# Kernel tuning notes

Measured on AMD Instinct MI355X. Metric: run time of the kernel, lower is better.

## Reference

```python
import jax, jax.numpy as jnp
import numpy as np

# Fixed genome topology (layered DAG, topologically ordered levels)
B = 4096      # batch
N_IN = 512    # input nodes
H1 = 1536     # hidden level 1
H2 = 1536     # hidden level 2
N_OUT = 512   # output nodes
FAN = 32      # fan-in per non-input node


def setup_inputs() -> dict:
    key = jax.random.key(0)
    ks = jax.random.split(key, 10)
    x = jax.random.normal(ks[0], (B, N_IN), dtype=jnp.float32)
    # level 1: sources among inputs [0, N_IN)
    src0 = jax.random.randint(ks[1], (H1 * FAN,), 0, N_IN, dtype=jnp.int32)
    dst0 = jax.random.randint(ks[2], (H1 * FAN,), 0, H1, dtype=jnp.int32)
    w0 = jax.random.normal(ks[3], (H1 * FAN,), dtype=jnp.float32) * 0.1
    # level 2: sources among inputs + level1 [0, N_IN+H1)
    src1 = jax.random.randint(ks[4], (H2 * FAN,), 0, N_IN + H1, dtype=jnp.int32)
    dst1 = jax.random.randint(ks[5], (H2 * FAN,), 0, H2, dtype=jnp.int32)
    w1 = jax.random.normal(ks[6], (H2 * FAN,), dtype=jnp.float32) * 0.1
    # output level: sources among all earlier nodes [0, N_IN+H1+H2)
    src2 = jax.random.randint(ks[7], (N_OUT * FAN,), 0, N_IN + H1 + H2, dtype=jnp.int32)
    dst2 = jax.random.randint(ks[8], (N_OUT * FAN,), 0, N_OUT, dtype=jnp.int32)
    w2 = jax.random.normal(ks[9], (N_OUT * FAN,), dtype=jnp.float32) * 0.1
    return dict(x=x, src0=src0, dst0=dst0, w0=w0,
                src1=src1, dst1=dst1, w1=w1,
                src2=src2, dst2=dst2, w2=w2)


def _level(node_values, src, dst, w, size):
    # per-edge weighted gather: [B, E]
    vals = node_values[:, src] * w
    # scatter-add into destination nodes of this level: [B, size]
    agg = jnp.zeros((node_values.shape[0], size), node_values.dtype).at[:, dst].add(vals)
    # per-node activation (genome.activation == 'relu'); relu(0)=0 matches
    # original's behavior of leaving unconnected nodes at zero
    return jax.nn.relu(agg)


def reference(x, src0, dst0, w0, src1, dst1, w1, src2, dst2, w2):
    nv = x                                        # [B, N_IN]
    h1 = _level(nv, src0, dst0, w0, H1)           # [B, H1]
    nv = jnp.concatenate([nv, h1], axis=1)        # [B, N_IN+H1]
    h2 = _level(nv, src1, dst1, w1, H2)           # [B, H2]
    nv = jnp.concatenate([nv, h2], axis=1)        # [B, N_IN+H1+H2]
    out = _level(nv, src2, dst2, w2, N_OUT)       # [B, N_OUT]
    return out
```

## Files before the change

### kernel.cpp

```cpp
#include <hip/hip_runtime.h>
#include <hip/hip_fp16.h>
#include <stdint.h>

#define BATCH 4096
#define N_IN  512
#define H1    1536
#define H2    1536
#define N_OUT 512
#define E0 (H1 * 32)
#define E1 (H2 * 32)
#define E2 (N_OUT * 32)
#define ETOT (E0 + E1 + E2)
#define NNODES (H1 + H2 + N_OUT)
#define MAXDEG 128

#define OFF_EDGES 33554432
#define OFF_CNT   (OFF_EDGES + (size_t)NNODES * MAXDEG * 8)

__global__ __launch_bounds__(256) void k_transpose_in(const float* __restrict__ x,
                                                      __half* __restrict__ xT) {
    __shared__ float tile[32][33];
    const int tx = threadIdx.x, ty = threadIdx.y;
    const int n0 = blockIdx.x * 32;
    const int b0 = blockIdx.y * 32;
#pragma unroll
    for (int k = 0; k < 32; k += 8)
        tile[ty + k][tx] = x[(size_t)(b0 + ty + k) * N_IN + (n0 + tx)];
    __syncthreads();
#pragma unroll
    for (int k = 0; k < 32; k += 8)
        xT[(size_t)(n0 + ty + k) * BATCH + (b0 + tx)] = __float2half_rn(tile[tx][ty + k]);
}

__global__ __launch_bounds__(256) void k_fill(const int* __restrict__ s0, const int* __restrict__ d0, const float* __restrict__ w0,
                                              const int* __restrict__ s1, const int* __restrict__ d1, const float* __restrict__ w1,
                                              const int* __restrict__ s2, const int* __restrict__ d2, const float* __restrict__ w2,
                                              int* __restrict__ cnt, int2* __restrict__ edges) {
    const int e = blockIdx.x * 256 + threadIdx.x;
    int src, node; float w;
    if (e < E0)           { src = s0[e];          node = d0[e];                w = w0[e]; }
    else if (e < E0 + E1) { int i = e - E0;       src = s1[i]; node = H1 + d1[i];        w = w1[i]; }
    else                  { int i = e - E0 - E1;  src = s2[i]; node = H1 + H2 + d2[i];   w = w2[i]; }
    const int pos = atomicAdd(&cnt[node], 1);
    if (pos < MAXDEG) edges[(size_t)node * MAXDEG + pos] = make_int2(src, __float_as_int(w));
}

__global__ __launch_bounds__(256) void k_pad(const int* __restrict__ cnt,
                                             int2* __restrict__ edges) {
    const int i = blockIdx.x * 256 + threadIdx.x;
    const int node = i >> 3, p = i & 7;
    if (node >= NNODES) return;
    int c = cnt[node];
    c = (c < 0) ? 0 : (c > MAXDEG - 8 ? MAXDEG - 8 : c);
    edges[(size_t)node * MAXDEG + c + p] = make_int2(0, 0);
}

__global__ __launch_bounds__(256, 2)
void k_level(const int2* __restrict__ edges,
             const int* __restrict__ cnt,
             const uint4* __restrict__ nv,
             uint4* __restrict__ outb) {
    const int tid  = threadIdx.x;
    const int lane = tid & 63, wv = tid >> 6;
    const int node = (blockIdx.y << 2) | wv;
    const int col8 = ((int)blockIdx.x << 6) | lane;

    int c = cnt[node];
    c = (c < 0) ? 0 : (c > MAXDEG - 8 ? MAXDEG - 8 : c);
    const int cp = (c + 7) & ~7;

    float a0 = 0.f, a1 = 0.f, a2 = 0.f, a3 = 0.f, a4 = 0.f, a5 = 0.f, a6 = 0.f, a7 = 0.f;
    const int2* slot = edges + (size_t)node * MAXDEG;

#define LOADK(k)                                                               \
    const int   s##k = __builtin_amdgcn_readlane(my.x, j + k) & 4095;          \
    const float w##k = __int_as_float(__builtin_amdgcn_readlane(my.y, j + k)); \
    const uint4 q##k = nv[((size_t)s##k << 9) | col8];

#define ACCK(k) {                                                  \
    const __half2* h = (const __half2*)&q##k;                      \
    a0 = fmaf(__low2float(h[0]),  w##k, a0);                       \
    a1 = fmaf(__high2float(h[0]), w##k, a1);                       \
    a2 = fmaf(__low2float(h[1]),  w##k, a2);                       \
    a3 = fmaf(__high2float(h[1]), w##k, a3);                       \
    a4 = fmaf(__low2float(h[2]),  w##k, a4);                       \
    a5 = fmaf(__high2float(h[2]), w##k, a5);                       \
    a6 = fmaf(__low2float(h[3]),  w##k, a6);                       \
    a7 = fmaf(__high2float(h[3]), w##k, a7); }

    for (int base = 0; base < cp; base += 64) {
        const int2 my = slot[base + lane];
        const int m = (cp - base < 64) ? (cp - base) : 64;
        for (int j = 0; j < m; j += 8) {
            LOADK(0) LOADK(1) LOADK(2) LOADK(3)
            LOADK(4) LOADK(5) LOADK(6) LOADK(7)
            ACCK(0) ACCK(1) ACCK(2) ACCK(3)
            ACCK(4) ACCK(5) ACCK(6) ACCK(7)
        }
    }
#undef LOADK
#undef ACCK

    a0 = fmaxf(a0, 0.f); a1 = fmaxf(a1, 0.f); a2 = fmaxf(a2, 0.f); a3 = fmaxf(a3, 0.f);
    a4 = fmaxf(a4, 0.f); a5 = fmaxf(a5, 0.f); a6 = fmaxf(a6, 0.f); a7 = fmaxf(a7, 0.f);

    const __half2 h0 = __floats2half2_rn(a0, a1);
    const __half2 h1 = __floats2half2_rn(a2, a3);
    const __half2 h2 = __floats2half2_rn(a4, a5);
    const __half2 h3 = __floats2half2_rn(a6, a7);
    uint4 p;
    p.x = *(const uint32_t*)&h0; p.y = *(const uint32_t*)&h1;
    p.z = *(const uint32_t*)&h2; p.w = *(const uint32_t*)&h3;
    outb[((size_t)node << 9) | col8] = p;
}

__global__ __launch_bounds__(256) void k_transpose_out(const __half* __restrict__ outh,
                                                       float* __restrict__ out) {
    __shared__ float tile[32][33];
    const int tx = threadIdx.x, ty = threadIdx.y;
    const int n0 = blockIdx.x * 32;
    const int b0 = blockIdx.y * 32;
#pragma unroll
    for (int k = 0; k < 32; k += 8)
        tile[ty + k][tx] = __half2float(outh[(size_t)(n0 + ty + k) * BATCH + (b0 + tx)]);
    __syncthreads();
#pragma unroll
    for (int k = 0; k < 32; k += 8)
        out[(size_t)(b0 + ty + k) * N_OUT + (n0 + tx)] = tile[tx][ty + k];
}

extern "C" void kernel_launch(void* const* d_in, const int* in_sizes, int n_in,
                              void* d_out, int out_size, void* d_ws, size_t ws_size,
                              hipStream_t stream) {
    const float* x  = (const float*)d_in[0];
    const int* s0   = (const int*)d_in[1];
    const int* dd0  = (const int*)d_in[2];
    const float* w0 = (const float*)d_in[3];
    const int* s1   = (const int*)d_in[4];
    const int* dd1  = (const int*)d_in[5];
    const float* w1 = (const float*)d_in[6];
    const int* s2   = (const int*)d_in[7];
    const int* dd2  = (const int*)d_in[8];
    const float* w2 = (const float*)d_in[9];

    char*   ws    = (char*)d_ws;
    __half* nvh   = (__half*)ws;
    uint4*  nv4   = (uint4*)ws;
    int2*   edges = (int2*)(ws + OFF_EDGES);
    int*    cnt   = (int*)(ws + OFF_CNT);

    hipMemsetAsync(cnt, 0, NNODES * sizeof(int), stream);
    k_fill<<<ETOT / 256, 256, 0, stream>>>(s0, dd0, w0, s1, dd1, w1, s2, dd2, w2, cnt, edges);
    k_pad<<<(NNODES * 8 + 255) / 256, 256, 0, stream>>>(cnt, edges);

    k_transpose_in<<<dim3(N_IN / 32, BATCH / 32), dim3(32, 8), 0, stream>>>(x, nvh);

    k_level<<<dim3(8, H1 / 4), 256, 0, stream>>>(edges, cnt, nv4,
                                                 nv4 + (size_t)N_IN * 512);
    k_level<<<dim3(8, H2 / 4), 256, 0, stream>>>(edges + (size_t)H1 * MAXDEG, cnt + H1, nv4,
                                                 nv4 + (size_t)(N_IN + H1) * 512);
    k_level<<<dim3(8, N_OUT / 4), 256, 0, stream>>>(edges + (size_t)(H1 + H2) * MAXDEG, cnt + H1 + H2, nv4,
                                                    nv4 + (size_t)(N_IN + H1 + H2) * 512);

    k_transpose_out<<<dim3(N_OUT / 32, BATCH / 32), dim3(32, 8), 0, stream>>>(
        (const __half*)(ws + (size_t)(N_IN + H1 + H2) * BATCH * 2), (float*)d_out);
}
```

Baseline: 151.4 us.

## Fuse all three levels into one batch-tiled kernel with node values in LDS

Replaces the transpose, per-level gather kernels and output transpose with a single kernel where each block owns 16 batch rows and keeps every node's fp16 values in shared memory across all three levels. Edges are packed into 32-bit words (16-bit source, fp16 weight) in fixed 80-slot rows, and the zero padding comes from memsetting the whole edge buffer. The intent is to remove the global-memory round trips for intermediate activations and the separate launches. In exchange, weights are rounded to fp16, in-degree is capped at 80, and the large LDS footprint (about 114 KB per block) limits occupancy and may cause bank conflicts on the gathered reads.

```diff
diff --git a/kernel.cpp b/kernel.cpp
--- a/kernel.cpp
+++ b/kernel.cpp
@@ -12,121 +12,96 @@
 #define E2 (N_OUT * 32)
 #define ETOT (E0 + E1 + E2)
 #define NNODES (H1 + H2 + N_OUT)
-#define MAXDEG 128
+#define PDEG 80
+#define C    16
 
-#define OFF_EDGES 33554432
-#define OFF_CNT   (OFF_EDGES + (size_t)NNODES * MAXDEG * 8)
+#define EDGE_BYTES ((size_t)NNODES * PDEG * 4)
+#define OFF_CNT    EDGE_BYTES
 
-__global__ __launch_bounds__(256) void k_transpose_in(const float* __restrict__ x,
-                                                      __half* __restrict__ xT) {
-    __shared__ float tile[32][33];
-    const int tx = threadIdx.x, ty = threadIdx.y;
-    const int n0 = blockIdx.x * 32;
-    const int b0 = blockIdx.y * 32;
-#pragma unroll
-    for (int k = 0; k < 32; k += 8)
-        tile[ty + k][tx] = x[(size_t)(b0 + ty + k) * N_IN + (n0 + tx)];
-    __syncthreads();
-#pragma unroll
-    for (int k = 0; k < 32; k += 8)
-        xT[(size_t)(n0 + ty + k) * BATCH + (b0 + tx)] = __float2half_rn(tile[tx][ty + k]);
+__global__ __launch_bounds__(256) void k_fill4(const int* __restrict__ s0, const int* __restrict__ d0, const float* __restrict__ w0,
+                                               const int* __restrict__ s1, const int* __restrict__ d1, const float* __restrict__ w1,
+                                               const int* __restrict__ s2, const int* __restrict__ d2, const float* __restrict__ w2,
+                                               int* __restrict__ cnt, uint32_t* __restrict__ edge4) {
+    const int e = blockIdx.x * 256 + threadIdx.x;
+    int src, node; float w;
+    if (e < E0)           { src = s0[e];          node = d0[e];                 w = w0[e]; }
+    else if (e < E0 + E1) { int i = e - E0;       src = s1[i]; node = H1 + d1[i];         w = w1[i]; }
+    else                  { int i = e - E0 - E1;  src = s2[i]; node = H1 + H2 + d2[i];    w = w2[i]; }
+    const int pos = atomicAdd(&cnt[node], 1);
+    if (pos < PDEG) {
+        const uint32_t hw = (uint32_t)__half_as_ushort(__float2half_rn(w));
+        edge4[(size_t)node * PDEG + pos] = ((uint32_t)src & 0xffffu) | (hw << 16);
+    }
 }
 
-__global__ __launch_bounds__(256) void k_fill(const int* __restrict__ s0, const int* __restrict__ d0, const float* __restrict__ w0,
-                                              const int* __restrict__ s1, const int* __restrict__ d1, const float* __restrict__ w1,
-                                              const int* __restrict__ s2, const int* __restrict__ d2, const float* __restrict__ w2,
-                                              int* __restrict__ cnt, int2* __restrict__ edges) {
-    const int e = blockIdx.x * 256 + threadIdx.x;
-    int src, node; float w;
-    if (e < E0)           { src = s0[e];          node = d0[e];                w = w0[e]; }
-    else if (e < E0 + E1) { int i = e - E0;       src = s1[i]; node = H1 + d1[i];        w = w1[i]; }
-    else                  { int i = e - E0 - E1;  src = s2[i]; node = H1 + H2 + d2[i];   w = w2[i]; }
-    const int pos = atomicAdd(&cnt[node], 1);
-    if (pos < MAXDEG) edges[(size_t)node * MAXDEG + pos] = make_int2(src, __float_as_int(w));
-}
+__global__ __launch_bounds__(512, 2)
+void k_net(const float* __restrict__ x,
+           const uint32_t* __restrict__ edge4,
+           const int* __restrict__ cnt,
+           float* __restrict__ out) {
+    __shared__ __half nvl[NNODES * C];
+    const int tid  = threadIdx.x;
+    const int b0   = blockIdx.x * C;
+    const int wave = tid >> 6, lane = tid & 63;
+    const int sub  = lane >> 3;
+    const int cp   = lane & 7;
 
-__global__ __launch_bounds__(256) void k_pad(const int* __restrict__ cnt,
-                                             int2* __restrict__ edges) {
-    const int i = blockIdx.x * 256 + threadIdx.x;
-    const int node = i >> 3, p = i & 7;
-    if (node >= NNODES) return;
-    int c = cnt[node];
-    c = (c < 0) ? 0 : (c > MAXDEG - 8 ? MAXDEG - 8 : c);
-    edges[(size_t)node * MAXDEG + c + p] = make_int2(0, 0);
-}
+#pragma unroll 4
+    for (int i = 0; i < C; ++i)
+        nvl[tid * C + i] = __float2half_rn(x[(size_t)(b0 + i) * N_IN + tid]);
+    __syncthreads();
 
-__global__ __launch_bounds__(256, 2)
-void k_level(const int2* __restrict__ edges,
-             const int* __restrict__ cnt,
-             const uint4* __restrict__ nv,
-             uint4* __restrict__ outb) {
-    const int tid  = threadIdx.x;
-    const int lane = tid & 63, wv = tid >> 6;
-    const int node = (blockIdx.y << 2) | wv;
-    const int col8 = ((int)blockIdx.x << 6) | lane;
+#pragma unroll 1
+    for (int l = 0; l < 3; ++l) {
+        const int nocts  = (l == 2) ? (N_OUT >> 3) : (H1 >> 3);
+        const int ebase  = (l == 0) ? 0 : (l == 1) ? H1 : (H1 + H2);
+        const int nvbase = (l == 0) ? N_IN : (N_IN + H1);
 
-    int c = cnt[node];
-    c = (c < 0) ? 0 : (c > MAXDEG - 8 ? MAXDEG - 8 : c);
-    const int cp = (c + 7) & ~7;
+        for (int o = wave; o < nocts; o += 8) {
+            const int ln   = (o << 3) | sub;
+            const int node = ebase + ln;
+            int c = cnt[node];
+            c = (c < 0) ? 0 : (c > PDEG ? PDEG : c);
+            int qm = c;
+#pragma unroll
+            for (int s = 8; s < 64; s += 8) {
+                const int oc = __builtin_amdgcn_readlane(c, s);
+                qm = (oc > qm) ? oc : qm;
+            }
+            qm = __builtin_amdgcn_readlane(qm, 0);
+            const int qmax = (qm + 7) & ~7;
 
-    float a0 = 0.f, a1 = 0.f, a2 = 0.f, a3 = 0.f, a4 = 0.f, a5 = 0.f, a6 = 0.f, a7 = 0.f;
-    const int2* slot = edges + (size_t)node * MAXDEG;
-
-#define LOADK(k)                                                               \
-    const int   s##k = __builtin_amdgcn_readlane(my.x, j + k) & 4095;          \
-    const float w##k = __int_as_float(__builtin_amdgcn_readlane(my.y, j + k)); \
-    const uint4 q##k = nv[((size_t)s##k << 9) | col8];
-
-#define ACCK(k) {                                                  \
-    const __half2* h = (const __half2*)&q##k;                      \
-    a0 = fmaf(__low2float(h[0]),  w##k, a0);                       \
-    a1 = fmaf(__high2float(h[0]), w##k, a1);                       \
-    a2 = fmaf(__low2float(h[1]),  w##k, a2);                       \
-    a3 = fmaf(__high2float(h[1]), w##k, a3);                       \
-    a4 = fmaf(__low2float(h[2]),  w##k, a4);                       \
-    a5 = fmaf(__high2float(h[2]), w##k, a5);                       \
-    a6 = fmaf(__low2float(h[3]),  w##k, a6);                       \
-    a7 = fmaf(__high2float(h[3]), w##k, a7); }
-
-    for (int base = 0; base < cp; base += 64) {
-        const int2 my = slot[base + lane];
-        const int m = (cp - base < 64) ? (cp - base) : 64;
-        for (int j = 0; j < m; j += 8) {
-            LOADK(0) LOADK(1) LOADK(2) LOADK(3)
-            LOADK(4) LOADK(5) LOADK(6) LOADK(7)
-            ACCK(0) ACCK(1) ACCK(2) ACCK(3)
-            ACCK(4) ACCK(5) ACCK(6) ACCK(7)
+            const uint32_t* __restrict__ row = edge4 + (size_t)node * PDEG;
+            float a0 = 0.f, a1 = 0.f;
+            uint4 e0 = *(const uint4*)(row);
+            uint4 e1 = *(const uint4*)(row + 4);
+            for (int j = 0; j < qmax; j += 8) {
+                const uint4 n0 = *(const uint4*)(row + j + 8);
+                const uint4 n1 = *(const uint4*)(row + j + 12);
+#define STEP(E) {                                                              \
+    const uint32_t ee = (E);                                                   \
+    const __half2 vv = *reinterpret_cast<const __half2*>(                      \
+        &nvl[(int)(ee & 0xffffu) * C + (cp << 1)]);                            \
+    const float wq = __high2float(*reinterpret_cast<const __half2*>(&ee));     \
+    a0 = fmaf(__low2float(vv),  wq, a0);                                       \
+    a1 = fmaf(__high2float(vv), wq, a1); }
+                STEP(e0.x) STEP(e0.y) STEP(e0.z) STEP(e0.w)
+                STEP(e1.x) STEP(e1.y) STEP(e1.z) STEP(e1.w)
+#undef STEP
+                e0 = n0; e1 = n1;
+            }
+            a0 = fmaxf(a0, 0.f);
+            a1 = fmaxf(a1, 0.f);
+            if (l < 2) {
+                *reinterpret_cast<__half2*>(&nvl[(nvbase + ln) * C + (cp << 1)]) =
+                    __floats2half2_rn(a0, a1);
+            } else {
+                out[(size_t)(b0 + (cp << 1))     * N_OUT + ln] = a0;
+                out[(size_t)(b0 + (cp << 1) + 1) * N_OUT + ln] = a1;
+            }
         }
+        __syncthreads();
     }
-#undef LOADK
-#undef ACCK
-
-    a0 = fmaxf(a0, 0.f); a1 = fmaxf(a1, 0.f); a2 = fmaxf(a2, 0.f); a3 = fmaxf(a3, 0.f);
-    a4 = fmaxf(a4, 0.f); a5 = fmaxf(a5, 0.f); a6 = fmaxf(a6, 0.f); a7 = fmaxf(a7, 0.f);
-
-    const __half2 h0 = __floats2half2_rn(a0, a1);
-    const __half2 h1 = __floats2half2_rn(a2, a3);
-    const __half2 h2 = __floats2half2_rn(a4, a5);
-    const __half2 h3 = __floats2half2_rn(a6, a7);
-    uint4 p;
-    p.x = *(const uint32_t*)&h0; p.y = *(const uint32_t*)&h1;
-    p.z = *(const uint32_t*)&h2; p.w = *(const uint32_t*)&h3;
-    outb[((size_t)node << 9) | col8] = p;
-}
-
-__global__ __launch_bounds__(256) void k_transpose_out(const __half* __restrict__ outh,
-                                                       float* __restrict__ out) {
-    __shared__ float tile[32][33];
-    const int tx = threadIdx.x, ty = threadIdx.y;
-    const int n0 = blockIdx.x * 32;
-    const int b0 = blockIdx.y * 32;
-#pragma unroll
-    for (int k = 0; k < 32; k += 8)
-        tile[ty + k][tx] = __half2float(outh[(size_t)(n0 + ty + k) * BATCH + (b0 + tx)]);
-    __syncthreads();
-#pragma unroll
-    for (int k = 0; k < 32; k += 8)
-        out[(size_t)(b0 + ty + k) * N_OUT + (n0 + tx)] = tile[tx][ty + k];
 }
 
 extern "C" void kernel_launch(void* const* d_in, const int* in_sizes, int n_in,
@@ -143,25 +118,12 @@
     const int* dd2  = (const int*)d_in[8];
     const float* w2 = (const float*)d_in[9];
 
-    char*   ws    = (char*)d_ws;
-    __half* nvh   = (__half*)ws;
-    uint4*  nv4   = (uint4*)ws;
-    int2*   edges = (int2*)(ws + OFF_EDGES);
-    int*    cnt   = (int*)(ws + OFF_CNT);
+    char*     ws    = (char*)d_ws;
+    uint32_t* edge4 = (uint32_t*)ws;
+    int*      cnt   = (int*)(ws + OFF_CNT);
 
-    hipMemsetAsync(cnt, 0, NNODES * sizeof(int), stream);
-    k_fill<<<ETOT / 256, 256, 0, stream>>>(s0, dd0, w0, s1, dd1, w1, s2, dd2, w2, cnt, edges);
-    k_pad<<<(NNODES * 8 + 255) / 256, 256, 0, stream>>>(cnt, edges);
+    hipMemsetAsync(ws, 0, EDGE_BYTES + NNODES * sizeof(int), stream);
+    k_fill4<<<ETOT / 256, 256, 0, stream>>>(s0, dd0, w0, s1, dd1, w1, s2, dd2, w2, cnt, edge4);
 
-    k_transpose_in<<<dim3(N_IN / 32, BATCH / 32), dim3(32, 8), 0, stream>>>(x, nvh);
-
-    k_level<<<dim3(8, H1 / 4), 256, 0, stream>>>(edges, cnt, nv4,
-                                                 nv4 + (size_t)N_IN * 512);
-    k_level<<<dim3(8, H2 / 4), 256, 0, stream>>>(edges + (size_t)H1 * MAXDEG, cnt + H1, nv4,
-                                                 nv4 + (size_t)(N_IN + H1) * 512);
-    k_level<<<dim3(8, N_OUT / 4), 256, 0, stream>>>(edges + (size_t)(H1 + H2) * MAXDEG, cnt + H1 + H2, nv4,
-                                                    nv4 + (size_t)(N_IN + H1 + H2) * 512);
-
-    k_transpose_out<<<dim3(N_OUT / 32, BATCH / 32), dim3(32, 8), 0, stream>>>(
-        (const __half*)(ws + (size_t)(N_IN + H1 + H2) * BATCH * 2), (float*)d_out);
+    k_net<<<BATCH / C, 512, 0, stream>>>(x, edge4, cnt, (float*)d_out);
 }
```

Result: slower. 215.8 us (+42.6%).
